# Performance work log

Measured on AMD Instinct MI355X. Metric: run time of the kernel, lower is better.

Reference implementation:

```python
import jax, jax.numpy as jnp
import numpy as np

W = 10        # hurst window == signature path window (increments)
DELTA_MAX = 1.5
BN_EPS = 1e-5


def _revcumsum(x, axis):
    return jnp.flip(jnp.cumsum(jnp.flip(x, axis), axis=axis), axis)


def _forward(features, hw1, hb1, hw2, hb2, hw3, hb3, gw1, gb1, gw2, gb2,
             p1, p1b, p2, p2b, p3, p3b, p4, p4b,
             w1, b1, gamma, beta, rmean, rvar, w2, b2, w3, b3):
    B, T, d = features.shape
    f32 = features.dtype
    # log returns, left-padded with 0
    lp = features[:, :, 0]
    ret = jnp.pad(lp[:, 1:] - lp[:, :-1], ((0, 0), (1, 0)))
    # Hurst estimator on sliding windows returns[:, t-W:t] for t in [W, T)
    idxh = jnp.arange(T - W)[:, None] + jnp.arange(W)[None, :]
    rw = ret[:, idxh]                                          # [B, T-W, W]
    hh = jax.nn.relu(rw @ hw1 + hb1)
    hh = jax.nn.relu(hh @ hw2 + hb2)
    H_tail = 0.5 * jax.nn.sigmoid((hh @ hw3 + hb3)[..., 0])    # [B, T-W]
    # first W entries copy the t=W estimate (matches torch slice-broadcast)
    H_local = jnp.concatenate([jnp.repeat(H_tail[:, :1], W, axis=1), H_tail], axis=1)
    vol = jnp.cumsum(jnp.abs(ret), axis=1) / (jnp.arange(1, T + 1, dtype=f32) + 1e-8)
    # depth gate from (H_local, vol_local)
    regime = jnp.stack([H_local, vol], axis=-1)                # [B, T, 2]
    gate = jax.nn.softmax(jax.nn.relu(regime @ gw1 + gb1) @ gw2 + gb2, axis=-1)  # [B,T,4]
    # windowed path increments: window at t covers global increments t-W .. t-1
    Dinc = features[:, 1:] - features[:, :-1]                  # [B, T-1, d]
    Dp = jnp.pad(Dinc, ((0, 0), (W, 0), (0, 0)))
    idx = jnp.arange(T)[:, None] + jnp.arange(W)[None, :]
    Dw = Dp[:, idx]                                            # [B, T, W, d] (zero-padded early)
    S = _revcumsum(Dw, 2)                                      # suffix sums S_r = sum_{m>=r} D_m
    lvl1 = S[:, :, 0]                                          # [B, T, d] = path[-1]-path[0]
    # level2 (torch loop) = sum_{i<=m} D_i (x) D_m  (diagonal included)
    A = Dw[..., :, None] * S[..., None, :]                     # [B, T, W, d, d]
    l2f = jnp.sum(A, axis=2).reshape(B, T, d * d)
    # level3 (torch loop) = sum_{i<j<=n} D_i (x) D_j (x) D_n
    RA = _revcumsum(A, 2) - A                                  # exclusive suffix sum of A
    l3f = jnp.einsum('btrd,btref->btdef', Dw, RA).reshape(B, T, d ** 3)
    # level4 = flatten(level2 (x) level2); (d^2)^2 == d^4 so no pad/trunc
    l4f = (l2f[..., :, None] * l2f[..., None, :]).reshape(B, T, d ** 4)
    proj1 = lvl1 @ p1 + p1b
    proj2 = jnp.concatenate([lvl1, l2f], -1) @ p2 + p2b
    proj3 = jnp.concatenate([lvl1, l2f, l3f], -1) @ p3 + p3b
    proj4 = jnp.concatenate([lvl1, l2f, l3f, l4f], -1) @ p4 + p4b
    # depth k active iff path_len >= k+1 i.e. t >= k (k = depth index)
    tv = jnp.arange(T)
    m2 = (tv >= 1).astype(f32)[None, :, None]
    m3 = (tv >= 2).astype(f32)[None, :, None]
    m4 = (tv >= 3).astype(f32)[None, :, None]
    sig_repr = (gate[..., 0:1] * proj1 + m2 * gate[..., 1:2] * proj2
                + m3 * gate[..., 2:3] * proj3 + m4 * gate[..., 3:4] * proj4)
    combined = jnp.concatenate([sig_repr, features], axis=-1)  # [B, T, h+d]
    h1 = jax.nn.relu(combined @ w1 + b1)
    bn = gamma * (h1 - rmean) * jax.lax.rsqrt(rvar + BN_EPS) + beta  # BatchNorm1d (eval)
    h2 = jax.nn.relu(bn @ w2 + b2)
    return DELTA_MAX * jnp.tanh((h2 @ w3 + b3)[..., 0])        # [B, T]


def setup_inputs() -> dict:
    key = jax.random.key(0)
    ks = jax.random.split(key, 24)
    B, T, d, h = 32, 2048, 5, 64
    def w(k, shape, s=0.1):
        return (jax.random.normal(k, shape) * s).astype(jnp.float32)
    z = lambda n: jnp.zeros((n,), jnp.float32)
    return dict(
        features=0.1 * jax.random.normal(ks[0], (B, T, d), jnp.float32),
        hw1=w(ks[1], (10, 32)), hb1=z(32),
        hw2=w(ks[2], (32, 32)), hb2=z(32),
        hw3=w(ks[3], (32, 1)), hb3=z(1),
        gw1=w(ks[4], (2, 32)), gb1=z(32),
        gw2=w(ks[5], (32, 4)), gb2=z(4),
        p1=w(ks[6], (5, h)), p1b=z(h),
        p2=w(ks[7], (30, h)), p2b=z(h),
        p3=w(ks[8], (155, h)), p3b=z(h),
        p4=w(ks[9], (780, h)), p4b=z(h),
        w1=w(ks[10], (h + d, h)), b1=z(h),
        gamma=jnp.ones((h,), jnp.float32), beta=z(h),
        rmean=0.05 * jax.random.normal(ks[11], (h,), dtype=jnp.float32),
        rvar=jax.random.uniform(ks[12], (h,), jnp.float32, 0.5, 1.5),
        w2=w(ks[13], (h, h // 2)), b2=z(h // 2),
        w3=w(ks[14], (h // 2, 1)), b3=z(1),
    )


def reference(features, hw1, hb1, hw2, hb2, hw3, hb3, gw1, gb1, gw2, gb2,
              p1, p1b, p2, p2b, p3, p3b, p4, p4b,
              w1, b1, gamma, beta, rmean, rvar, w2, b2, w3, b3):
    return _forward(features, hw1, hb1, hw2, hb2, hw3, hb3, gw1, gb1, gw2, gb2,
                    p1, p1b, p2, p2b, p3, p3b, p4, p4b,
                    w1, b1, gamma, beta, rmean, rvar, w2, b2, w3, b3)
```

## Files before the change

kernel.cpp:

```cpp
#include <hip/hip_runtime.h>
#include <math.h>

#define TT 2048
#define W 10

typedef short bf16x8 __attribute__((ext_vector_type(8)));
typedef float f32x4 __attribute__((ext_vector_type(4)));

__device__ __forceinline__ unsigned short f32_bf16(float f) {
  unsigned int u = __float_as_uint(f);
  u = (u + 0x7fffu + ((u >> 16) & 1u)) >> 16;
  return (unsigned short)u;
}
__device__ __forceinline__ float bf16_f32(unsigned short h) {
  return __uint_as_float(((unsigned int)h) << 16);
}

__device__ __forceinline__ void wstore(unsigned short* WtH, unsigned short* WtL,
                                       int g, float v) {
  unsigned short hi = f32_bf16(v);
  WtH[g] = hi;
  WtL[g] = f32_bf16(v - bf16_f32(hi));
}

__global__ __launch_bounds__(256) void wprep_kernel(
    const float* __restrict__ p1, const float* __restrict__ p2,
    const float* __restrict__ p3, const float* __restrict__ p4,
    unsigned short* __restrict__ WtH, unsigned short* __restrict__ WtL) {
  int g = blockIdx.x * 256 + threadIdx.x;
  if (g < 2048) {
    int h = g / 32, k = g % 32;
    wstore(WtH, WtL, g, (k < 5) ? p1[k * 64 + h] : 0.f);
  } else if (g < 4096) {
    int loc = g - 2048, h = loc / 32, k = loc % 32;
    wstore(WtH, WtL, g, (k < 30) ? p2[k * 64 + h] : 0.f);
  } else if (g < 14336) {
    int loc = g - 4096, h = loc / 160, k = loc % 160;
    wstore(WtH, WtL, g, (k < 155) ? p3[k * 64 + h] : 0.f);
  } else {
    int loc = g - 14336, h = loc / 800, k = loc % 800;
    wstore(WtH, WtL, g, (k < 780) ? p4[k * 64 + h] : 0.f);
  }
}

__global__ __launch_bounds__(256) void prep_kernel(const float* __restrict__ F,
                                                   float* __restrict__ ret,
                                                   float* __restrict__ vol) {
  __shared__ float sAbs[TT];
  __shared__ float sPart[256];
  const int b = blockIdx.x, tid = threadIdx.x;
  const float* fb = F + (size_t)b * TT * 5;
#pragma unroll
  for (int u = 0; u < 8; ++u) {
    int t = u * 256 + tid;
    float rv = 0.f;
    if (t > 0) rv = fb[t * 5] - fb[(t - 1) * 5];
    ret[b * TT + t] = rv;
    sAbs[t] = fabsf(rv);
  }
  __syncthreads();
  float loc[8];
  float run = 0.f;
#pragma unroll
  for (int u = 0; u < 8; ++u) { run += sAbs[tid * 8 + u]; loc[u] = run; }
  sPart[tid] = run;
  __syncthreads();
  for (int off = 1; off < 256; off <<= 1) {
    float v = (tid >= off) ? sPart[tid - off] : 0.f;
    __syncthreads();
    sPart[tid] += v;
    __syncthreads();
  }
  float excl = sPart[tid] - run;
#pragma unroll
  for (int u = 0; u < 8; ++u) {
    int t = tid * 8 + u;
    vol[b * TT + t] = (excl + loc[u]) / ((float)(t + 1) + 1e-8f);
  }
}

__global__ __launch_bounds__(256) void gate_kernel(
    const float* __restrict__ ret, const float* __restrict__ vol,
    const float* __restrict__ hw1, const float* __restrict__ hb1,
    const float* __restrict__ hw2, const float* __restrict__ hb2,
    const float* __restrict__ hw3, const float* __restrict__ hb3,
    const float* __restrict__ gw1, const float* __restrict__ gb1,
    const float* __restrict__ gw2, const float* __restrict__ gb2,
    float* __restrict__ gate) {
  const int pos = blockIdx.x * 256 + threadIdx.x;
  const int t = pos & (TT - 1);
  const int start = (t >= W) ? (t - W) : 0;
  const float* rp = ret + (pos - t) + start;
  float r[W];
#pragma unroll
  for (int u = 0; u < W; ++u) r[u] = rp[u];
  float h1v[32];
#pragma unroll
  for (int j = 0; j < 32; ++j) {
    float a = hb1[j];
#pragma unroll
    for (int u = 0; u < W; ++u) a = fmaf(r[u], hw1[u * 32 + j], a);
    h1v[j] = fmaxf(a, 0.f);
  }
  float hs = hb3[0];
#pragma unroll
  for (int j = 0; j < 32; ++j) {
    float a = hb2[j];
#pragma unroll
    for (int u = 0; u < 32; ++u) a = fmaf(h1v[u], hw2[u * 32 + j], a);
    hs = fmaf(fmaxf(a, 0.f), hw3[j], hs);
  }
  const float H = 0.5f / (1.f + expf(-hs));
  const float vv = vol[pos];
  float l0 = gb2[0], l1 = gb2[1], l2 = gb2[2], l3 = gb2[3];
#pragma unroll
  for (int j = 0; j < 32; ++j) {
    float z = fmaxf(fmaf(H, gw1[j], fmaf(vv, gw1[32 + j], gb1[j])), 0.f);
    l0 = fmaf(z, gw2[j * 4 + 0], l0);
    l1 = fmaf(z, gw2[j * 4 + 1], l1);
    l2 = fmaf(z, gw2[j * 4 + 2], l2);
    l3 = fmaf(z, gw2[j * 4 + 3], l3);
  }
  float m = fmaxf(fmaxf(l0, l1), fmaxf(l2, l3));
  float e0 = expf(l0 - m), e1 = expf(l1 - m), e2 = expf(l2 - m), e3 = expf(l3 - m);
  float inv = 1.f / (e0 + e1 + e2 + e3);
  ((float4*)gate)[pos] = make_float4(e0 * inv, e1 * inv, e2 * inv, e3 * inv);
}

#define MFMA16(a, b, c) __builtin_amdgcn_mfma_f32_16x16x32_bf16((a), (b), (c), 0, 0, 0)

__global__ __launch_bounds__(256, 2) void sig_kernel(
    const float* __restrict__ F, const float* __restrict__ gate,
    const unsigned short* __restrict__ WtH, const unsigned short* __restrict__ WtL,
    const float* __restrict__ p1b, const float* __restrict__ p2b,
    const float* __restrict__ p3b, const float* __restrict__ p4b,
    const float* __restrict__ w1, const float* __restrict__ b1,
    const float* __restrict__ gam, const float* __restrict__ bet,
    const float* __restrict__ rmean, const float* __restrict__ rvar,
    const float* __restrict__ w2, const float* __restrict__ b2,
    const float* __restrict__ w3, const float* __restrict__ b3,
    float* __restrict__ out) {
  __shared__ unsigned short phiH[16][808];
  __shared__ unsigned short phiL[16][808];
  __shared__ float sUnion[2128];
  __shared__ float sFeat[80];

  float* sDw = sUnion;
  float* sS = sUnion + 800;
  float* sL2 = sUnion + 1600;

  const int tid = threadIdx.x;
  const int posBase = blockIdx.x * 16;

  for (int u = tid; u < 800; u += 256) {
    int p = u / 50, rr = u % 50;
    int r = rr / 5, i = rr % 5;
    int pos = posBase + p;
    int t = pos & (TT - 1);
    int q = t + r - W;
    float dv = 0.f;
    if (q >= 0) {
      const float* fb = F + (size_t)(pos - t) * 5;
      dv = fb[(q + 1) * 5 + i] - fb[q * 5 + i];
    }
    sDw[u] = dv;
  }
  for (int u = tid; u < 80; u += 256) sFeat[u] = F[(size_t)posBase * 5 + u];
  __syncthreads();

  for (int u = tid; u < 80; u += 256) {
    int p = u / 5, i = u % 5;
    float s = 0.f;
#pragma unroll
    for (int r = W - 1; r >= 0; --r) {
      s += sDw[p * 50 + r * 5 + i];
      sS[p * 50 + r * 5 + i] = s;
    }
    unsigned short hi = f32_bf16(s);
    phiH[p][i] = hi;
    phiL[p][i] = f32_bf16(s - bf16_f32(hi));
  }
  __syncthreads();

  for (int u = tid; u < 400; u += 256) {
    int p = u / 25, ef = u % 25;
    int e = ef / 5, fi = ef % 5;
    const float* dwp = sDw + p * 50;
    const float* sp = sS + p * 50;
    float a = 0.f;
    float l3a[5] = {0.f, 0.f, 0.f, 0.f, 0.f};
#pragma unroll
    for (int r = W - 1; r >= 0; --r) {
      float aa = a;
#pragma unroll
      for (int i = 0; i < 5; ++i) l3a[i] = fmaf(dwp[r * 5 + i], aa, l3a[i]);
      a = fmaf(dwp[r * 5 + e], sp[r * 5 + fi], a);
    }
    sL2[p * 25 + ef] = a;
    unsigned short hi = f32_bf16(a);
    phiH[p][5 + ef] = hi;
    phiL[p][5 + ef] = f32_bf16(a - bf16_f32(hi));
#pragma unroll
    for (int i = 0; i < 5; ++i) {
      int kk = 30 + i * 25 + ef;
      unsigned short h2i = f32_bf16(l3a[i]);
      phiH[p][kk] = h2i;
      phiL[p][kk] = f32_bf16(l3a[i] - bf16_f32(h2i));
    }
  }
  __syncthreads();

  for (int u = tid; u < 16 * 625; u += 256) {
    int p = u / 625, a2 = u % 625;
    float v = sL2[p * 25 + a2 / 25] * sL2[p * 25 + a2 % 25];
    int kk = 155 + a2;
    unsigned short hi = f32_bf16(v);
    phiH[p][kk] = hi;
    phiL[p][kk] = f32_bf16(v - bf16_f32(hi));
  }
  for (int u = tid; u < 16 * 28; u += 256) {
    int p = u / 28, kk = 780 + u % 28;
    phiH[p][kk] = 0;
    phiL[p][kk] = 0;
  }
  __syncthreads();

  const int lane = tid & 63, wv = tid >> 6;
  const int col = lane & 15, quad = lane >> 4;
  const int hw = wv * 16;

  const unsigned short* a4H = WtH + 14336 + (hw + col) * 800 + quad * 8;
  const unsigned short* a4L = WtL + 14336 + (hw + col) * 800 + quad * 8;
  const unsigned short* a3H = WtH + 4096 + (hw + col) * 160 + quad * 8;
  const unsigned short* a3L = WtL + 4096 + (hw + col) * 160 + quad * 8;
  const unsigned short* a2H = WtH + 2048 + (hw + col) * 32 + quad * 8;
  const unsigned short* a2L = WtL + 2048 + (hw + col) * 32 + quad * 8;
  const unsigned short* a1H = WtH + 0 + (hw + col) * 32 + quad * 8;
  const unsigned short* a1L = WtL + 0 + (hw + col) * 32 + quad * 8;
  const unsigned short* bH = &phiH[col][quad * 8];
  const unsigned short* bL = &phiL[col][quad * 8];

  f32x4 acc4a = {0.f, 0.f, 0.f, 0.f}, acc4b = {0.f, 0.f, 0.f, 0.f};
  f32x4 acc3a = {0.f, 0.f, 0.f, 0.f}, acc3b = {0.f, 0.f, 0.f, 0.f};
  f32x4 acc2 = {0.f, 0.f, 0.f, 0.f}, acc1 = {0.f, 0.f, 0.f, 0.f};

  for (int s = 0; s < 25; ++s) {
    bf16x8 bh = *(const bf16x8*)(bH + s * 32);
    bf16x8 bl = *(const bf16x8*)(bL + s * 32);
    bf16x8 ah = *(const bf16x8*)(a4H + s * 32);
    bf16x8 al = *(const bf16x8*)(a4L + s * 32);
    acc4a = MFMA16(ah, bh, acc4a);
    acc4b = MFMA16(ah, bl, acc4b);
    acc4b = MFMA16(al, bh, acc4b);
    if (s < 5) {
      bf16x8 ch = *(const bf16x8*)(a3H + s * 32);
      bf16x8 cl = *(const bf16x8*)(a3L + s * 32);
      acc3a = MFMA16(ch, bh, acc3a);
      acc3b = MFMA16(ch, bl, acc3b);
      acc3b = MFMA16(cl, bh, acc3b);
      if (s == 0) {
        bf16x8 dh = *(const bf16x8*)a2H;
        bf16x8 dl = *(const bf16x8*)a2L;
        acc2 = MFMA16(dh, bh, acc2);
        acc2 = MFMA16(dh, bl, acc2);
        acc2 = MFMA16(dl, bh, acc2);
        bf16x8 eh = *(const bf16x8*)a1H;
        bf16x8 el = *(const bf16x8*)a1L;
        acc1 = MFMA16(eh, bh, acc1);
        acc1 = MFMA16(eh, bl, acc1);
        acc1 = MFMA16(el, bh, acc1);
      }
    }
  }

  float* sSig = sUnion;
  float* sBn = sUnion + 1088;
  {
    f32x4 a4 = acc4a + acc4b;
    f32x4 a3 = acc3a + acc3b;
    const int pl = col;
    const int pos = posBase + pl;
    const int t = pos & (TT - 1);
    float4 g = ((const float4*)gate)[pos];
    float g0 = g.x;
    float g1 = (t >= 1) ? g.y : 0.f;
    float g2 = (t >= 2) ? g.z : 0.f;
    float g3 = (t >= 3) ? g.w : 0.f;
#pragma unroll
    for (int r = 0; r < 4; ++r) {
      int h = hw + quad * 4 + r;
      float v = g0 * (acc1[r] + p1b[h]) + g1 * (acc2[r] + p2b[h]) +
                g2 * (a3[r] + p3b[h]) + g3 * (a4[r] + p4b[h]);
      sSig[pl * 68 + h] = v;
    }
  }
  __syncthreads();

  {
    const int j = lane;
    float a0 = b1[j];
    float a1 = a0, a2 = a0, a3 = a0;
    const float* sg0 = sSig + (wv * 4 + 0) * 68;
    const float* sg1 = sSig + (wv * 4 + 1) * 68;
    const float* sg2 = sSig + (wv * 4 + 2) * 68;
    const float* sg3 = sSig + (wv * 4 + 3) * 68;
    for (int i = 0; i < 64; ++i) {
      float wt = w1[i * 64 + j];
      a0 = fmaf(sg0[i], wt, a0);
      a1 = fmaf(sg1[i], wt, a1);
      a2 = fmaf(sg2[i], wt, a2);
      a3 = fmaf(sg3[i], wt, a3);
    }
    const float* ft = sFeat + wv * 4 * 5;
#pragma unroll
    for (int i = 0; i < 5; ++i) {
      float wt = w1[(64 + i) * 64 + j];
      a0 = fmaf(ft[i], wt, a0);
      a1 = fmaf(ft[5 + i], wt, a1);
      a2 = fmaf(ft[10 + i], wt, a2);
      a3 = fmaf(ft[15 + i], wt, a3);
    }
    float sc = gam[j] * rsqrtf(rvar[j] + 1e-5f);
    float rm = rmean[j], be = bet[j];
    sBn[(wv * 4 + 0) * 65 + j] = fmaf(fmaxf(a0, 0.f) - rm, sc, be);
    sBn[(wv * 4 + 1) * 65 + j] = fmaf(fmaxf(a1, 0.f) - rm, sc, be);
    sBn[(wv * 4 + 2) * 65 + j] = fmaf(fmaxf(a2, 0.f) - rm, sc, be);
    sBn[(wv * 4 + 3) * 65 + j] = fmaf(fmaxf(a3, 0.f) - rm, sc, be);
  }
  __syncthreads();

  const float b3s = b3[0];
  for (int task = tid; task < 512; task += 256) {
    int p = task >> 5, k = task & 31;
    const float* bnp = sBn + p * 65;
    float a = b2[k];
    for (int j = 0; j < 64; ++j) a = fmaf(bnp[j], w2[j * 32 + k], a);
    float partial = fmaxf(a, 0.f) * w3[k];
#pragma unroll
    for (int off = 16; off >= 1; off >>= 1) partial += __shfl_xor(partial, off, 32);
    if (k == 0) out[posBase + p] = 1.5f * tanhf(partial + b3s);
  }
}

extern "C" void kernel_launch(void* const* d_in, const int* in_sizes, int n_in,
                              void* d_out, int out_size, void* d_ws, size_t ws_size,
                              hipStream_t stream) {
  const float* F = (const float*)d_in[0];
  const float* hw1 = (const float*)d_in[1];
  const float* hb1 = (const float*)d_in[2];
  const float* hw2 = (const float*)d_in[3];
  const float* hb2 = (const float*)d_in[4];
  const float* hw3 = (const float*)d_in[5];
  const float* hb3 = (const float*)d_in[6];
  const float* gw1 = (const float*)d_in[7];
  const float* gb1 = (const float*)d_in[8];
  const float* gw2 = (const float*)d_in[9];
  const float* gb2 = (const float*)d_in[10];
  const float* p1 = (const float*)d_in[11];
  const float* p1b = (const float*)d_in[12];
  const float* p2 = (const float*)d_in[13];
  const float* p2b = (const float*)d_in[14];
  const float* p3 = (const float*)d_in[15];
  const float* p3b = (const float*)d_in[16];
  const float* p4 = (const float*)d_in[17];
  const float* p4b = (const float*)d_in[18];
  const float* w1 = (const float*)d_in[19];
  const float* b1 = (const float*)d_in[20];
  const float* gam = (const float*)d_in[21];
  const float* bet = (const float*)d_in[22];
  const float* rmean = (const float*)d_in[23];
  const float* rvar = (const float*)d_in[24];
  const float* w2 = (const float*)d_in[25];
  const float* b2 = (const float*)d_in[26];
  const float* w3 = (const float*)d_in[27];
  const float* b3 = (const float*)d_in[28];

  float* ws = (float*)d_ws;
  float* ret = ws;
  float* vol = ws + 65536;
  float* gate = ws + 131072;
  unsigned short* WtH = (unsigned short*)(ws + 393216);
  unsigned short* WtL = WtH + 65536;
  float* out = (float*)d_out;

  wprep_kernel<<<256, 256, 0, stream>>>(p1, p2, p3, p4, WtH, WtL);
  prep_kernel<<<32, 256, 0, stream>>>(F, ret, vol);
  gate_kernel<<<256, 256, 0, stream>>>(ret, vol, hw1, hb1, hw2, hb2, hw3, hb3,
                                       gw1, gb1, gw2, gb2, gate);
  sig_kernel<<<4096, 256, 0, stream>>>(F, gate, WtH, WtL, p1b, p2b, p3b, p4b,
                                       w1, b1, gam, bet, rmean, rvar, w2, b2,
                                       w3, b3, out);
}
```

Baseline: 265.8 us.

## Fuse prep kernels and split signature MFMA K-loop across 512 threads

Merges the weight-prep, return/volatility prep and gate kernels into a single launch, recomputing the per-batch prefix scan in each block so ret and vol never round-trip through global memory. The signature kernel now runs with 512 threads, and the level-4 MFMA reduction is split between two wave groups whose partial sums are combined through shared memory. The level-4 outer-product fill is vectorised with packed two-element stores, and bf16 hi/lo splitting switches to truncation. The cost is extra block-level syncs and a redundant scan per prep block, and truncation changes rounding slightly.

```diff
diff --git a/kernel.cpp b/kernel.cpp
--- a/kernel.cpp
+++ b/kernel.cpp
@@ -7,62 +7,69 @@
 typedef short bf16x8 __attribute__((ext_vector_type(8)));
 typedef float f32x4 __attribute__((ext_vector_type(4)));
 
-__device__ __forceinline__ unsigned short f32_bf16(float f) {
-  unsigned int u = __float_as_uint(f);
-  u = (u + 0x7fffu + ((u >> 16) & 1u)) >> 16;
-  return (unsigned short)u;
+__device__ __forceinline__ void splitTrunc(float v, unsigned short& hi,
+                                           unsigned short& lo) {
+  unsigned int u = __float_as_uint(v);
+  hi = (unsigned short)(u >> 16);
+  float r = v - __uint_as_float(u & 0xffff0000u);
+  lo = (unsigned short)(__float_as_uint(r) >> 16);
 }
-__device__ __forceinline__ float bf16_f32(unsigned short h) {
-  return __uint_as_float(((unsigned int)h) << 16);
-}
-
-__device__ __forceinline__ void wstore(unsigned short* WtH, unsigned short* WtL,
-                                       int g, float v) {
-  unsigned short hi = f32_bf16(v);
-  WtH[g] = hi;
-  WtL[g] = f32_bf16(v - bf16_f32(hi));
-}
-
-__global__ __launch_bounds__(256) void wprep_kernel(
+
+__global__ __launch_bounds__(256) void pre_kernel(
+    const float* __restrict__ F,
+    const float* __restrict__ hw1, const float* __restrict__ hb1,
+    const float* __restrict__ hw2, const float* __restrict__ hb2,
+    const float* __restrict__ hw3, const float* __restrict__ hb3,
+    const float* __restrict__ gw1, const float* __restrict__ gb1,
+    const float* __restrict__ gw2, const float* __restrict__ gb2,
     const float* __restrict__ p1, const float* __restrict__ p2,
     const float* __restrict__ p3, const float* __restrict__ p4,
-    unsigned short* __restrict__ WtH, unsigned short* __restrict__ WtL) {
-  int g = blockIdx.x * 256 + threadIdx.x;
-  if (g < 2048) {
-    int h = g / 32, k = g % 32;
-    wstore(WtH, WtL, g, (k < 5) ? p1[k * 64 + h] : 0.f);
-  } else if (g < 4096) {
-    int loc = g - 2048, h = loc / 32, k = loc % 32;
-    wstore(WtH, WtL, g, (k < 30) ? p2[k * 64 + h] : 0.f);
-  } else if (g < 14336) {
-    int loc = g - 4096, h = loc / 160, k = loc % 160;
-    wstore(WtH, WtL, g, (k < 155) ? p3[k * 64 + h] : 0.f);
-  } else {
-    int loc = g - 14336, h = loc / 800, k = loc % 800;
-    wstore(WtH, WtL, g, (k < 780) ? p4[k * 64 + h] : 0.f);
-  }
-}
-
-__global__ __launch_bounds__(256) void prep_kernel(const float* __restrict__ F,
-                                                   float* __restrict__ ret,
-                                                   float* __restrict__ vol) {
-  __shared__ float sAbs[TT];
+    unsigned short* __restrict__ WtH, unsigned short* __restrict__ WtL,
+    float* __restrict__ gate) {
+  const int bid = blockIdx.x;
+  const int tid = threadIdx.x;
+  if (bid >= 256) {
+    int g = (bid - 256) * 256 + tid;
+    float v;
+    if (g < 2048) {
+      int h = g >> 5, k = g & 31;
+      v = (k < 5) ? p1[k * 64 + h] : 0.f;
+    } else if (g < 4096) {
+      int loc = g - 2048, h = loc >> 5, k = loc & 31;
+      v = (k < 30) ? p2[k * 64 + h] : 0.f;
+    } else if (g < 14336) {
+      int loc = g - 4096, h = loc / 160, k = loc - h * 160;
+      v = (k < 155) ? p3[k * 64 + h] : 0.f;
+    } else {
+      int loc = g - 14336, h = loc / 800, k = loc - h * 800;
+      if (k < 155) v = p4[k * 64 + h];
+      else if (k >= 160 && k < 785) v = p4[(k - 5) * 64 + h];
+      else v = 0.f;
+    }
+    unsigned short hi, lo;
+    splitTrunc(v, hi, lo);
+    WtH[g] = hi;
+    WtL[g] = lo;
+    return;
+  }
+  __shared__ float sRet[TT];
+  __shared__ float sCum[TT];
   __shared__ float sPart[256];
-  const int b = blockIdx.x, tid = threadIdx.x;
+  const int b = bid >> 3;
+  const int t0 = (bid & 7) << 8;
   const float* fb = F + (size_t)b * TT * 5;
 #pragma unroll
   for (int u = 0; u < 8; ++u) {
     int t = u * 256 + tid;
-    float rv = 0.f;
-    if (t > 0) rv = fb[t * 5] - fb[(t - 1) * 5];
-    ret[b * TT + t] = rv;
-    sAbs[t] = fabsf(rv);
-  }
-  __syncthreads();
-  float loc[8];
-  float run = 0.f;
-#pragma unroll
-  for (int u = 0; u < 8; ++u) { run += sAbs[tid * 8 + u]; loc[u] = run; }
+    sRet[t] = (t > 0) ? (fb[t * 5] - fb[(t - 1) * 5]) : 0.f;
+  }
+  __syncthreads();
+  float loc8[8], run = 0.f;
+#pragma unroll
+  for (int u = 0; u < 8; ++u) {
+    run += fabsf(sRet[tid * 8 + u]);
+    loc8[u] = run;
+  }
   sPart[tid] = run;
   __syncthreads();
   for (int off = 1; off < 256; off <<= 1) {
@@ -73,27 +80,14 @@
   }
   float excl = sPart[tid] - run;
 #pragma unroll
-  for (int u = 0; u < 8; ++u) {
-    int t = tid * 8 + u;
-    vol[b * TT + t] = (excl + loc[u]) / ((float)(t + 1) + 1e-8f);
-  }
-}
-
-__global__ __launch_bounds__(256) void gate_kernel(
-    const float* __restrict__ ret, const float* __restrict__ vol,
-    const float* __restrict__ hw1, const float* __restrict__ hb1,
-    const float* __restrict__ hw2, const float* __restrict__ hb2,
-    const float* __restrict__ hw3, const float* __restrict__ hb3,
-    const float* __restrict__ gw1, const float* __restrict__ gb1,
-    const float* __restrict__ gw2, const float* __restrict__ gb2,
-    float* __restrict__ gate) {
-  const int pos = blockIdx.x * 256 + threadIdx.x;
-  const int t = pos & (TT - 1);
+  for (int u = 0; u < 8; ++u) sCum[tid * 8 + u] = excl + loc8[u];
+  __syncthreads();
+  const int t = t0 + tid;
+  const float vv = sCum[t] / ((float)(t + 1) + 1e-8f);
   const int start = (t >= W) ? (t - W) : 0;
-  const float* rp = ret + (pos - t) + start;
   float r[W];
 #pragma unroll
-  for (int u = 0; u < W; ++u) r[u] = rp[u];
+  for (int u = 0; u < W; ++u) r[u] = sRet[start + u];
   float h1v[32];
 #pragma unroll
   for (int j = 0; j < 32; ++j) {
@@ -111,7 +105,6 @@
     hs = fmaf(fmaxf(a, 0.f), hw3[j], hs);
   }
   const float H = 0.5f / (1.f + expf(-hs));
-  const float vv = vol[pos];
   float l0 = gb2[0], l1 = gb2[1], l2 = gb2[2], l3 = gb2[3];
 #pragma unroll
   for (int j = 0; j < 32; ++j) {
@@ -122,14 +115,15 @@
     l3 = fmaf(z, gw2[j * 4 + 3], l3);
   }
   float m = fmaxf(fmaxf(l0, l1), fmaxf(l2, l3));
-  float e0 = expf(l0 - m), e1 = expf(l1 - m), e2 = expf(l2 - m), e3 = expf(l3 - m);
+  float e0 = expf(l0 - m), e1 = expf(l1 - m), e2 = expf(l2 - m),
+        e3 = expf(l3 - m);
   float inv = 1.f / (e0 + e1 + e2 + e3);
-  ((float4*)gate)[pos] = make_float4(e0 * inv, e1 * inv, e2 * inv, e3 * inv);
+  ((float4*)gate)[b * TT + t] = make_float4(e0 * inv, e1 * inv, e2 * inv, e3 * inv);
 }
 
 #define MFMA16(a, b, c) __builtin_amdgcn_mfma_f32_16x16x32_bf16((a), (b), (c), 0, 0, 0)
 
-__global__ __launch_bounds__(256, 2) void sig_kernel(
+__global__ __launch_bounds__(512, 4) void sig_kernel(
     const float* __restrict__ F, const float* __restrict__ gate,
     const unsigned short* __restrict__ WtH, const unsigned short* __restrict__ WtL,
     const float* __restrict__ p1b, const float* __restrict__ p2b,
@@ -142,19 +136,19 @@
     float* __restrict__ out) {
   __shared__ unsigned short phiH[16][808];
   __shared__ unsigned short phiL[16][808];
-  __shared__ float sUnion[2128];
+  __shared__ __align__(16) float sX[3152];
   __shared__ float sFeat[80];
 
-  float* sDw = sUnion;
-  float* sS = sUnion + 800;
-  float* sL2 = sUnion + 1600;
+  float* sDw = sX;
+  float* sS = sX + 800;
+  float* sL2 = sX + 1600;
 
   const int tid = threadIdx.x;
   const int posBase = blockIdx.x * 16;
 
-  for (int u = tid; u < 800; u += 256) {
-    int p = u / 50, rr = u % 50;
-    int r = rr / 5, i = rr % 5;
+  for (int u = tid; u < 800; u += 512) {
+    int p = u / 50, rr = u - p * 50;
+    int r = rr / 5, i = rr - r * 5;
     int pos = posBase + p;
     int t = pos & (TT - 1);
     int q = t + r - W;
@@ -165,26 +159,27 @@
     }
     sDw[u] = dv;
   }
-  for (int u = tid; u < 80; u += 256) sFeat[u] = F[(size_t)posBase * 5 + u];
-  __syncthreads();
-
-  for (int u = tid; u < 80; u += 256) {
-    int p = u / 5, i = u % 5;
+  if (tid < 80) sFeat[tid] = F[(size_t)posBase * 5 + tid];
+  __syncthreads();
+
+  if (tid < 80) {
+    int p = tid / 5, i = tid - (tid / 5) * 5;
     float s = 0.f;
 #pragma unroll
     for (int r = W - 1; r >= 0; --r) {
       s += sDw[p * 50 + r * 5 + i];
       sS[p * 50 + r * 5 + i] = s;
     }
-    unsigned short hi = f32_bf16(s);
+    unsigned short hi, lo;
+    splitTrunc(s, hi, lo);
     phiH[p][i] = hi;
-    phiL[p][i] = f32_bf16(s - bf16_f32(hi));
-  }
-  __syncthreads();
-
-  for (int u = tid; u < 400; u += 256) {
-    int p = u / 25, ef = u % 25;
-    int e = ef / 5, fi = ef % 5;
+    phiL[p][i] = lo;
+  }
+  __syncthreads();
+
+  if (tid < 400) {
+    int p = tid / 25, ef = tid - (tid / 25) * 25;
+    int e = ef / 5, fi = ef - e * 5;
     const float* dwp = sDw + p * 50;
     const float* sp = sS + p * 50;
     float a = 0.f;
@@ -197,144 +192,184 @@
       a = fmaf(dwp[r * 5 + e], sp[r * 5 + fi], a);
     }
     sL2[p * 25 + ef] = a;
-    unsigned short hi = f32_bf16(a);
+    unsigned short hi, lo;
+    splitTrunc(a, hi, lo);
     phiH[p][5 + ef] = hi;
-    phiL[p][5 + ef] = f32_bf16(a - bf16_f32(hi));
+    phiL[p][5 + ef] = lo;
 #pragma unroll
     for (int i = 0; i < 5; ++i) {
-      int kk = 30 + i * 25 + ef;
-      unsigned short h2i = f32_bf16(l3a[i]);
-      phiH[p][kk] = h2i;
-      phiL[p][kk] = f32_bf16(l3a[i] - bf16_f32(h2i));
-    }
-  }
-  __syncthreads();
-
-  for (int u = tid; u < 16 * 625; u += 256) {
-    int p = u / 625, a2 = u % 625;
-    float v = sL2[p * 25 + a2 / 25] * sL2[p * 25 + a2 % 25];
-    int kk = 155 + a2;
-    unsigned short hi = f32_bf16(v);
-    phiH[p][kk] = hi;
-    phiL[p][kk] = f32_bf16(v - bf16_f32(hi));
-  }
-  for (int u = tid; u < 16 * 28; u += 256) {
-    int p = u / 28, kk = 780 + u % 28;
+      splitTrunc(l3a[i], hi, lo);
+      phiH[p][30 + i * 25 + ef] = hi;
+      phiL[p][30 + i * 25 + ef] = lo;
+    }
+  }
+  if (tid < 320) {
+    int p = tid / 20, mm = tid - (tid / 20) * 20;
+    int kk = (mm < 5) ? (155 + mm) : (780 + mm);
     phiH[p][kk] = 0;
     phiL[p][kk] = 0;
   }
   __syncthreads();
 
-  const int lane = tid & 63, wv = tid >> 6;
+  {
+    int p = tid >> 5, t32 = tid & 31;
+    int base = t32 * 20;
+    int count = (t32 == 31) ? 5 : 20;
+    const float* l2p = sL2 + p * 25;
+    int i = base / 25, j = base - i * 25;
+    unsigned short* rowH = &phiH[p][160 + base];
+    unsigned short* rowL = &phiL[p][160 + base];
+    int mEnd = count & ~1;
+    for (int m = 0; m < mEnd; m += 2) {
+      float v0 = l2p[i] * l2p[j];
+      j++; if (j == 25) { j = 0; i++; }
+      float v1 = l2p[i] * l2p[j];
+      j++; if (j == 25) { j = 0; i++; }
+      unsigned short h0, lo0, h1, lo1;
+      splitTrunc(v0, h0, lo0);
+      splitTrunc(v1, h1, lo1);
+      *(unsigned int*)(rowH + m) = (unsigned int)h0 | ((unsigned int)h1 << 16);
+      *(unsigned int*)(rowL + m) = (unsigned int)lo0 | ((unsigned int)lo1 << 16);
+    }
+    if (count & 1) {
+      float v0 = l2p[i] * l2p[j];
+      unsigned short h0, lo0;
+      splitTrunc(v0, h0, lo0);
+      rowH[mEnd] = h0;
+      rowL[mEnd] = lo0;
+    }
+  }
+  __syncthreads();
+
+  const int lane = tid & 63;
+  const int wvAll = tid >> 6;
+  const int ht = wvAll & 3, kg = wvAll >> 2;
   const int col = lane & 15, quad = lane >> 4;
-  const int hw = wv * 16;
-
-  const unsigned short* a4H = WtH + 14336 + (hw + col) * 800 + quad * 8;
-  const unsigned short* a4L = WtL + 14336 + (hw + col) * 800 + quad * 8;
-  const unsigned short* a3H = WtH + 4096 + (hw + col) * 160 + quad * 8;
-  const unsigned short* a3L = WtL + 4096 + (hw + col) * 160 + quad * 8;
-  const unsigned short* a2H = WtH + 2048 + (hw + col) * 32 + quad * 8;
-  const unsigned short* a2L = WtL + 2048 + (hw + col) * 32 + quad * 8;
-  const unsigned short* a1H = WtH + 0 + (hw + col) * 32 + quad * 8;
-  const unsigned short* a1L = WtL + 0 + (hw + col) * 32 + quad * 8;
-  const unsigned short* bH = &phiH[col][quad * 8];
-  const unsigned short* bL = &phiL[col][quad * 8];
+  const int hw = ht * 16;
+  const int arow = hw + col;
+
+  const unsigned short* bHp = &phiH[col][quad * 8];
+  const unsigned short* bLp = &phiL[col][quad * 8];
+  const unsigned short* a4H = WtH + 14336 + arow * 800 + quad * 8;
+  const unsigned short* a4L = WtL + 14336 + arow * 800 + quad * 8;
 
   f32x4 acc4a = {0.f, 0.f, 0.f, 0.f}, acc4b = {0.f, 0.f, 0.f, 0.f};
   f32x4 acc3a = {0.f, 0.f, 0.f, 0.f}, acc3b = {0.f, 0.f, 0.f, 0.f};
   f32x4 acc2 = {0.f, 0.f, 0.f, 0.f}, acc1 = {0.f, 0.f, 0.f, 0.f};
 
-  for (int s = 0; s < 25; ++s) {
-    bf16x8 bh = *(const bf16x8*)(bH + s * 32);
-    bf16x8 bl = *(const bf16x8*)(bL + s * 32);
-    bf16x8 ah = *(const bf16x8*)(a4H + s * 32);
-    bf16x8 al = *(const bf16x8*)(a4L + s * 32);
-    acc4a = MFMA16(ah, bh, acc4a);
-    acc4b = MFMA16(ah, bl, acc4b);
-    acc4b = MFMA16(al, bh, acc4b);
-    if (s < 5) {
+  if (kg == 0) {
+    for (int s = 0; s < 16; ++s) {
+      bf16x8 bh = *(const bf16x8*)(bHp + s * 32);
+      bf16x8 bl = *(const bf16x8*)(bLp + s * 32);
+      bf16x8 ah = *(const bf16x8*)(a4H + s * 32);
+      bf16x8 al = *(const bf16x8*)(a4L + s * 32);
+      acc4a = MFMA16(ah, bh, acc4a);
+      acc4b = MFMA16(ah, bl, acc4b);
+      acc4b = MFMA16(al, bh, acc4b);
+    }
+  } else {
+    for (int s = 16; s < 25; ++s) {
+      bf16x8 bh = *(const bf16x8*)(bHp + s * 32);
+      bf16x8 bl = *(const bf16x8*)(bLp + s * 32);
+      bf16x8 ah = *(const bf16x8*)(a4H + s * 32);
+      bf16x8 al = *(const bf16x8*)(a4L + s * 32);
+      acc4a = MFMA16(ah, bh, acc4a);
+      acc4b = MFMA16(ah, bl, acc4b);
+      acc4b = MFMA16(al, bh, acc4b);
+    }
+    const unsigned short* a3H = WtH + 4096 + arow * 160 + quad * 8;
+    const unsigned short* a3L = WtL + 4096 + arow * 160 + quad * 8;
+    for (int s = 0; s < 5; ++s) {
+      bf16x8 bh = *(const bf16x8*)(bHp + s * 32);
+      bf16x8 bl = *(const bf16x8*)(bLp + s * 32);
       bf16x8 ch = *(const bf16x8*)(a3H + s * 32);
       bf16x8 cl = *(const bf16x8*)(a3L + s * 32);
       acc3a = MFMA16(ch, bh, acc3a);
       acc3b = MFMA16(ch, bl, acc3b);
       acc3b = MFMA16(cl, bh, acc3b);
-      if (s == 0) {
-        bf16x8 dh = *(const bf16x8*)a2H;
-        bf16x8 dl = *(const bf16x8*)a2L;
-        acc2 = MFMA16(dh, bh, acc2);
-        acc2 = MFMA16(dh, bl, acc2);
-        acc2 = MFMA16(dl, bh, acc2);
-        bf16x8 eh = *(const bf16x8*)a1H;
-        bf16x8 el = *(const bf16x8*)a1L;
-        acc1 = MFMA16(eh, bh, acc1);
-        acc1 = MFMA16(eh, bl, acc1);
-        acc1 = MFMA16(el, bh, acc1);
-      }
-    }
-  }
-
-  float* sSig = sUnion;
-  float* sBn = sUnion + 1088;
-  {
+    }
+    bf16x8 bh0 = *(const bf16x8*)(bHp);
+    bf16x8 bl0 = *(const bf16x8*)(bLp);
+    const unsigned short* a2H = WtH + 2048 + arow * 32 + quad * 8;
+    const unsigned short* a2L = WtL + 2048 + arow * 32 + quad * 8;
+    bf16x8 dh = *(const bf16x8*)a2H;
+    bf16x8 dl = *(const bf16x8*)a2L;
+    acc2 = MFMA16(dh, bh0, acc2);
+    acc2 = MFMA16(dh, bl0, acc2);
+    acc2 = MFMA16(dl, bh0, acc2);
+    const unsigned short* a1H = WtH + arow * 32 + quad * 8;
+    const unsigned short* a1L = WtL + arow * 32 + quad * 8;
+    bf16x8 eh = *(const bf16x8*)a1H;
+    bf16x8 el = *(const bf16x8*)a1L;
+    acc1 = MFMA16(eh, bh0, acc1);
+    acc1 = MFMA16(eh, bl0, acc1);
+    acc1 = MFMA16(el, bh0, acc1);
+  }
+
+  const int pos = posBase + col;
+  const int t = pos & (TT - 1);
+  float4 g = ((const float4*)gate)[pos];
+  const float g0 = g.x;
+  const float g1 = (t >= 1) ? g.y : 0.f;
+  const float g2 = (t >= 2) ? g.z : 0.f;
+  const float g3 = (t >= 3) ? g.w : 0.f;
+
+  if (kg == 1) {
     f32x4 a4 = acc4a + acc4b;
     f32x4 a3 = acc3a + acc3b;
-    const int pl = col;
-    const int pos = posBase + pl;
-    const int t = pos & (TT - 1);
-    float4 g = ((const float4*)gate)[pos];
-    float g0 = g.x;
-    float g1 = (t >= 1) ? g.y : 0.f;
-    float g2 = (t >= 2) ? g.z : 0.f;
-    float g3 = (t >= 3) ? g.w : 0.f;
+    f32x4 v;
+#pragma unroll
+    for (int r = 0; r < 4; ++r)
+      v[r] = g0 * acc1[r] + g1 * acc2[r] + g2 * a3[r] + g3 * a4[r];
+    *(f32x4*)&sX[(ht * 64 + lane) * 4] = v;
+  }
+  __syncthreads();
+  if (kg == 0) {
+    f32x4 a4 = acc4a + acc4b;
+    f32x4 vo = *(const f32x4*)&sX[(ht * 64 + lane) * 4];
+    float* sSig = sX + 1024;
 #pragma unroll
     for (int r = 0; r < 4; ++r) {
       int h = hw + quad * 4 + r;
-      float v = g0 * (acc1[r] + p1b[h]) + g1 * (acc2[r] + p2b[h]) +
-                g2 * (a3[r] + p3b[h]) + g3 * (a4[r] + p4b[h]);
-      sSig[pl * 68 + h] = v;
+      float bias = g0 * p1b[h] + g1 * p2b[h] + g2 * p3b[h] + g3 * p4b[h];
+      sSig[col * 68 + h] = vo[r] + g3 * a4[r] + bias;
     }
   }
   __syncthreads();
 
   {
+    const float* sSig = sX + 1024;
+    float* sBn = sX + 2112;
     const int j = lane;
-    float a0 = b1[j];
-    float a1 = a0, a2 = a0, a3 = a0;
-    const float* sg0 = sSig + (wv * 4 + 0) * 68;
-    const float* sg1 = sSig + (wv * 4 + 1) * 68;
-    const float* sg2 = sSig + (wv * 4 + 2) * 68;
-    const float* sg3 = sSig + (wv * 4 + 3) * 68;
+    const int pA = wvAll * 2, pB = pA + 1;
+    float a0 = b1[j], a1 = a0;
+    const float* sg0 = sSig + pA * 68;
+    const float* sg1 = sSig + pB * 68;
     for (int i = 0; i < 64; ++i) {
       float wt = w1[i * 64 + j];
       a0 = fmaf(sg0[i], wt, a0);
       a1 = fmaf(sg1[i], wt, a1);
-      a2 = fmaf(sg2[i], wt, a2);
-      a3 = fmaf(sg3[i], wt, a3);
-    }
-    const float* ft = sFeat + wv * 4 * 5;
+    }
 #pragma unroll
     for (int i = 0; i < 5; ++i) {
       float wt = w1[(64 + i) * 64 + j];
-      a0 = fmaf(ft[i], wt, a0);
-      a1 = fmaf(ft[5 + i], wt, a1);
-      a2 = fmaf(ft[10 + i], wt, a2);
-      a3 = fmaf(ft[15 + i], wt, a3);
+      a0 = fmaf(sFeat[pA * 5 + i], wt, a0);
+      a1 = fmaf(sFeat[pB * 5 + i], wt, a1);
     }
     float sc = gam[j] * rsqrtf(rvar[j] + 1e-5f);
     float rm = rmean[j], be = bet[j];
-    sBn[(wv * 4 + 0) * 65 + j] = fmaf(fmaxf(a0, 0.f) - rm, sc, be);
-    sBn[(wv * 4 + 1) * 65 + j] = fmaf(fmaxf(a1, 0.f) - rm, sc, be);
-    sBn[(wv * 4 + 2) * 65 + j] = fmaf(fmaxf(a2, 0.f) - rm, sc, be);
-    sBn[(wv * 4 + 3) * 65 + j] = fmaf(fmaxf(a3, 0.f) - rm, sc, be);
-  }
-  __syncthreads();
-
-  const float b3s = b3[0];
-  for (int task = tid; task < 512; task += 256) {
-    int p = task >> 5, k = task & 31;
+    sBn[pA * 65 + j] = fmaf(fmaxf(a0, 0.f) - rm, sc, be);
+    sBn[pB * 65 + j] = fmaf(fmaxf(a1, 0.f) - rm, sc, be);
+  }
+  __syncthreads();
+
+  {
+    const float* sBn = sX + 2112;
+    const float b3s = b3[0];
+    int p = tid >> 5, k = tid & 31;
     const float* bnp = sBn + p * 65;
     float a = b2[k];
-    for (int j = 0; j < 64; ++j) a = fmaf(bnp[j], w2[j * 32 + k], a);
+    for (int jj = 0; jj < 64; ++jj) a = fmaf(bnp[jj], w2[jj * 32 + k], a);
     float partial = fmaxf(a, 0.f) * w3[k];
 #pragma unroll
     for (int off = 16; off >= 1; off >>= 1) partial += __shfl_xor(partial, off, 32);
@@ -376,18 +411,15 @@
   const float* b3 = (const float*)d_in[28];
 
   float* ws = (float*)d_ws;
-  float* ret = ws;
-  float* vol = ws + 65536;
-  float* gate = ws + 131072;
-  unsigned short* WtH = (unsigned short*)(ws + 393216);
+  float* gate = ws;
+  unsigned short* WtH = (unsigned short*)(ws + 262144);
   unsigned short* WtL = WtH + 65536;
   float* out = (float*)d_out;
 
-  wprep_kernel<<<256, 256, 0, stream>>>(p1, p2, p3, p4, WtH, WtL);
-  prep_kernel<<<32, 256, 0, stream>>>(F, ret, vol);
-  gate_kernel<<<256, 256, 0, stream>>>(ret, vol, hw1, hb1, hw2, hb2, hw3, hb3,
-                                       gw1, gb1, gw2, gb2, gate);
-  sig_kernel<<<4096, 256, 0, stream>>>(F, gate, WtH, WtL, p1b, p2b, p3b, p4b,
+  pre_kernel<<<512, 256, 0, stream>>>(F, hw1, hb1, hw2, hb2, hw3, hb3, gw1,
+                                      gb1, gw2, gb2, p1, p2, p3, p4, WtH, WtL,
+                                      gate);
+  sig_kernel<<<4096, 512, 0, stream>>>(F, gate, WtH, WtL, p1b, p2b, p3b, p4b,
                                        w1, b1, gam, bet, rmean, rvar, w2, b2,
                                        w3, b3, out);
 }
```

New measurement: 245.7 us. -7.6%, faster.
